# Performance work log

Hardware: AMD Instinct MI355X
Metric: run time of the kernel (lower is better)

The kernel has to match this reference:

```python
import jax, jax.numpy as jnp
import numpy as np
from jax import lax

B, L, H, I, Z = 1024, 128, 256, 32, 128  # batch, max_length, hidden, input_size, latent


def setup_inputs() -> dict:
    key = jax.random.key(0)
    ks = jax.random.split(key, 32)
    p = lambda k, shape: (jax.random.normal(k, shape, dtype=jnp.float32) * 0.05)
    d = {
        "x": jax.random.normal(ks[0], (B, Z), dtype=jnp.float32),
        "W1": p(ks[1], (512, Z)), "b1": p(ks[2], (512,)),
        "W2": p(ks[3], (512, 512)), "b2": p(ks[4], (512,)),
        "W3": p(ks[5], (512, 512)), "b3": p(ks[6], (512,)),
        # predict_h / predict_c / predict_x_0 heads
        "Wh1": p(ks[7], (512, 512)), "bh1": p(ks[8], (512,)),
        "Wh2": p(ks[9], (H, 512)), "bh2": p(ks[10], (H,)),
        "Wc1": p(ks[11], (512, 512)), "bc1": p(ks[12], (512,)),
        "Wc2": p(ks[13], (H, 512)), "bc2": p(ks[14], (H,)),
        "Wx1": p(ks[15], (512, 512)), "bx1": p(ks[16], (512,)),
        "Wx2": p(ks[17], (H, 512)), "bx2": p(ks[18], (H,)),
        # decode LSTM (input H -> hidden H), PyTorch gate order i,f,g,o
        "rWih": p(ks[19], (4 * H, H)), "rWhh": p(ks[20], (4 * H, H)),
        "rbih": p(ks[21], (4 * H,)), "rbhh": p(ks[22], (4 * H,)),
        # predictor LSTM (input H -> hidden I)
        "pWih": p(ks[23], (4 * I, H)), "pWhh": p(ks[24], (4 * I, I)),
        "pbih": p(ks[25], (4 * I,)), "pbhh": p(ks[26], (4 * I,)),
    }
    return d


def _leaky(v):
    return jnp.where(v >= 0, v, 0.2 * v)


def _lstm_cell(xt, h, c, Wih, Whh, b):
    gates = xt @ Wih.T + h @ Whh.T + b  # [B, 4G]
    i, f, g, o = jnp.split(gates, 4, axis=-1)
    c_new = jax.nn.sigmoid(f) * c + jax.nn.sigmoid(i) * jnp.tanh(g)
    h_new = jax.nn.sigmoid(o) * jnp.tanh(c_new)
    return h_new, c_new


def _forward(x, W1, b1, W2, b2, W3, b3, Wh1, bh1, Wh2, bh2, Wc1, bc1, Wc2, bc2,
             Wx1, bx1, Wx2, bx2, rWih, rWhh, rbih, rbhh, pWih, pWhh, pbih, pbhh):
    t = _leaky(x @ W1.T + b1)
    t = _leaky(t @ W2.T + b2)
    t = _leaky(t @ W3.T + b3)
    h = _leaky(t @ Wh1.T + bh1) @ Wh2.T + bh2   # [B, H]
    c = _leaky(t @ Wc1.T + bc1) @ Wc2.T + bc2   # [B, H]
    x0 = _leaky(t @ Wx1.T + bx1) @ Wx2.T + bx2  # [B, H]

    rb = rbih + rbhh
    # The torch loop re-feeds the growing sequence through the LSTM from the
    # same initial (h, c) each step; deterministically this equals a single
    # O(L) self-feeding scan: token_{i} = h-output of step i, fed at step i+1.
    def dec_step(carry, _):
        tok, hh, cc = carry
        h2, c2 = _lstm_cell(tok, hh, cc, rWih, rWhh, rb)
        return (h2, h2, c2), h2

    _, outs = lax.scan(dec_step, (x0, h, c), None, length=L)  # [L, B, H]

    pb = pbih + pbhh
    def pred_step(carry, xt):
        hh, cc = carry
        hh, cc = _lstm_cell(xt, hh, cc, pWih, pWhh, pb)
        return (hh, cc), hh

    h0 = jnp.zeros((B, I), dtype=x.dtype)
    _, pouts = lax.scan(pred_step, (h0, h0), outs)  # [L, B, I]
    y = jnp.transpose(pouts, (1, 0, 2))  # [B, L, I]

    layer_type = jax.nn.softmax(y[..., : I - 1], axis=-1)
    features = jax.nn.sigmoid(y[..., I - 1:])
    return jnp.concatenate([layer_type, features], axis=-1)


def reference(x, W1, b1, W2, b2, W3, b3, Wh1, bh1, Wh2, bh2, Wc1, bc1, Wc2, bc2,
              Wx1, bx1, Wx2, bx2, rWih, rWhh, rbih, rbhh, pWih, pWhh, pbih, pbhh):
    return _forward(x, W1, b1, W2, b2, W3, b3, Wh1, bh1, Wh2, bh2, Wc1, bc1, Wc2, bc2,
                    Wx1, bx1, Wx2, bx2, rWih, rWhh, rbih, rbhh, pWih, pWhh, pbih, pbhh)
```

## Files before the change

kernel.cpp:

```cpp
#include <hip/hip_runtime.h>
#include <hip/hip_fp8.h>

typedef unsigned short u16;
typedef unsigned char u8;
typedef __attribute__((ext_vector_type(8))) __bf16 bfrag;
typedef long long f8frag;
typedef __attribute__((ext_vector_type(4))) float f32x4;

static __device__ __forceinline__ f32x4 MFMA(bfrag a, bfrag b, f32x4 c) {
  return __builtin_amdgcn_mfma_f32_16x16x32_bf16(a, b, c, 0, 0, 0);
}
static __device__ __forceinline__ f32x4 MFMA8(f8frag a, f8frag b, f32x4 c) {
  return __builtin_amdgcn_mfma_f32_16x16x32_fp8_fp8(a, b, c, 0, 0, 0);
}

static __device__ __forceinline__ u16 f2b(float f) {
  union { float f; unsigned u; } v; v.f = f;
  unsigned r = (v.u + 0x7fffu + ((v.u >> 16) & 1u)) >> 16;
  return (u16)r;
}
static __device__ __forceinline__ u8 f2e4m3(float f) {
  return (u8)(__builtin_amdgcn_cvt_pk_fp8_f32(f, f, 0, false) & 0xff);
}
static __device__ __forceinline__ unsigned pk4_e4m3(float a, float b, float c, float d) {
  int p = __builtin_amdgcn_cvt_pk_fp8_f32(a, b, 0, false);
  p = __builtin_amdgcn_cvt_pk_fp8_f32(c, d, p, true);
  return (unsigned)p;
}
static __device__ __forceinline__ float rcp(float x) { return __builtin_amdgcn_rcpf(x); }
static __device__ __forceinline__ float ssig(float x) {
  float E = __expf(x);
  return E * rcp(1.f + E);
}
static __device__ __forceinline__ float2 lstm2(float gi, float gf, float gg,
                                               float go, float c) {
  float Ei = __expf(gi), Ef = __expf(gf), Eg = __expf(2.f * gg), Eo = __expf(go);
  float P = 1.f + Ef, Q = 1.f + Ei, R = 1.f + Eg;
  float QR = Q * R;
  float num = c * Ef * QR + Ei * P * (Eg - 1.f);
  float cn = num * rcp(P * QR);
  float Ec = __expf(2.f * cn);
  float hn = Eo * (Ec - 1.f) * rcp((1.f + Eo) * (Ec + 1.f));
  return make_float2(hn, cn);
}

#define LDS_BARRIER() asm volatile("s_waitcnt lgkmcnt(0)\ns_barrier" ::: "memory")
#define PIN_A8(A) asm volatile("" : "+a"(A[0]), "+a"(A[1]), "+a"(A[2]), "+a"(A[3]), \
                                    "+a"(A[4]), "+a"(A[5]), "+a"(A[6]), "+a"(A[7]))
#define PIN_V8(A) asm volatile("" : "+v"(A[0]), "+v"(A[1]), "+v"(A[2]), "+v"(A[3]), \
                                    "+v"(A[4]), "+v"(A[5]), "+v"(A[6]), "+v"(A[7]))

struct PrepArgs {
  const float *x, *W1, *W2, *W3, *Wh1, *Wc1, *Wx1, *Wh2, *Wc2, *Wx2;
  const float *rWih, *rWhh, *rbih, *rbhh, *pWih, *pWhh, *pbih, *pbhh;
  u16 *Xbf, *W1b, *W2b, *W3b, *Wh1b, *Wc1b, *Wx1b, *Wh2b, *Wc2b, *Wx2b;
  u16 *WcatR;
  u8 *WsS, *pWsS, *pWhhS;
  float *rbR, *pbR;
  unsigned *flags;
};

static __device__ __forceinline__ void emit_stream(u16* dst, const float* src,
                                                   int i, int K, int ktbits) {
  int j = i & 7, lane = (i >> 3) & 63;
  int kt = (i >> 9) & ((1 << ktbits) - 1);
  int nt = (i >> (9 + ktbits)) & 3;
  int ct = i >> (11 + ktbits);
  int srow = ct * 64 + nt * 16 + (lane & 15);
  int scol = kt * 32 + ((lane >> 4) & 3) * 8 + j;
  dst[i] = f2b(src[srow * K + scol]);
}

__global__ __launch_bounds__(256) void prep(PrepArgs p) {
  const int tid0 = blockIdx.x * 256 + threadIdx.x;
  const int stride = gridDim.x * 256;
  switch (blockIdx.y) {
    case 0: for (int i = tid0; i < 131072; i += stride) p.Xbf[i] = f2b(p.x[i]); break;
    case 1: for (int i = tid0; i < 65536;  i += stride) emit_stream(p.W1b, p.W1, i, 128, 2); break;
    case 2: for (int i = tid0; i < 262144; i += stride) emit_stream(p.W2b, p.W2, i, 512, 4); break;
    case 3: for (int i = tid0; i < 262144; i += stride) emit_stream(p.W3b, p.W3, i, 512, 4); break;
    case 4: for (int i = tid0; i < 262144; i += stride) emit_stream(p.Wh1b, p.Wh1, i, 512, 4); break;
    case 5: for (int i = tid0; i < 262144; i += stride) emit_stream(p.Wc1b, p.Wc1, i, 512, 4); break;
    case 6: for (int i = tid0; i < 262144; i += stride) emit_stream(p.Wx1b, p.Wx1, i, 512, 4); break;
    case 7: for (int i = tid0; i < 131072; i += stride) emit_stream(p.Wh2b, p.Wh2, i, 512, 4); break;
    case 8: for (int i = tid0; i < 131072; i += stride) emit_stream(p.Wc2b, p.Wc2, i, 512, 4); break;
    case 9: for (int i = tid0; i < 131072; i += stride) emit_stream(p.Wx2b, p.Wx2, i, 512, 4); break;
    case 10:
      for (int i = tid0; i < 524288; i += stride) {
        int j = i & 7, lane = (i >> 3) & 63, kt = (i >> 9) & 15;
        int gate = (i >> 13) & 3, w16 = i >> 15;
        int srow = gate * 256 + w16 * 16 + (lane & 15);
        int k = kt * 32 + ((lane >> 4) & 3) * 8 + j;
        float v = (k < 256) ? p.rWih[srow * 256 + k] : p.rWhh[srow * 256 + (k - 256)];
        p.WcatR[i] = f2b(v);
      }
      break;
    case 11:
      for (int i = tid0; i < 1024; i += stride) {
        int srow = (((i >> 4) & 3) << 8) + ((i >> 6) << 4) + (i & 15);
        p.rbR[i] = p.rbih[srow] + p.rbhh[srow];
      }
      break;
    case 12:
      for (int i = tid0; i < 32768; i += stride) {
        int j = i & 7, lane = (i >> 3) & 63, kt = (i >> 9) & 7, w = i >> 12;
        int n = w * 16 + (lane & 15);
        int srow = ((n & 3) << 5) + (n >> 2);
        int k = kt * 32 + ((lane >> 4) & 3) * 8 + j;
        p.pWsS[i] = f2e4m3(p.pWih[srow * 256 + k]);
      }
      break;
    case 13:
      for (int i = tid0; i < 4096; i += stride) {
        int j = i & 7, lane = (i >> 3) & 63, w = i >> 9;
        int n = w * 16 + (lane & 15);
        int srow = ((n & 3) << 5) + (n >> 2);
        int k = ((lane >> 4) & 3) * 8 + j;
        p.pWhhS[i] = f2e4m3(p.pWhh[srow * 32 + k]);
      }
      break;
    case 14:
      for (int i = tid0; i < 128; i += stride) {
        int srow = ((i & 3) << 5) + (i >> 2);
        p.pbR[i] = p.pbih[srow] + p.pbhh[srow];
      }
      for (int i = tid0; i < 64; i += stride)
        __hip_atomic_store(p.flags + i, 0u, __ATOMIC_RELAXED, __HIP_MEMORY_SCOPE_AGENT);
      break;
    case 15:
      for (int i = tid0; i < 262144; i += stride) {
        int j = i & 7, lane = (i >> 3) & 63, kt = (i >> 9) & 7;
        int gate = (i >> 12) & 3, g16 = i >> 14;
        int srow = gate * 256 + g16 * 16 + (lane & 15);
        int k = kt * 32 + ((lane >> 4) & 3) * 8 + j;
        p.WsS[i] = f2e4m3(p.rWih[srow * 256 + k] + p.rWhh[srow * 256 + k]);
      }
      break;
  }
}

__global__ __launch_bounds__(256) void gemm_act(
    const u16* __restrict__ X, const u16* __restrict__ W,
    const float* __restrict__ bias,
    u16* __restrict__ Yb, float* __restrict__ Yf,
    int K, int ldo, int coloff, int leaky) {
  const int rt = blockIdx.x, ct = blockIdx.y;
  const int lane = threadIdx.x & 63, wave = threadIdx.x >> 6;
  const int m15 = lane & 15, q = lane >> 4, kq = q * 8;
  const int KT = K >> 5;
  const int row = rt * 64 + wave * 16 + m15;
  f32x4 acc[4] = {};
  const u16* xp = X + (size_t)row * K + kq;
  const u16* wst = W + lane * 8;
  for (int kt = 0; kt < KT; kt++) {
    bfrag a = *(const bfrag*)(xp + kt * 32);
#pragma unroll
    for (int nt = 0; nt < 4; nt++) {
      const u16* wp = wst + (size_t)((ct * 4 + nt) * KT + kt) * 512;
      acc[nt] = MFMA(a, *(const bfrag*)wp, acc[nt]);
    }
  }
#pragma unroll
  for (int nt = 0; nt < 4; nt++) {
    int col = ct * 64 + nt * 16 + m15;
    float bv = bias[col];
#pragma unroll
    for (int r = 0; r < 4; r++) {
      int orow = rt * 64 + wave * 16 + q * 4 + r;
      float v = acc[nt][r] + bv;
      if (leaky) v = v >= 0.f ? v : 0.2f * v;
      if (Yb) Yb[(size_t)orow * ldo + coloff + col] = f2b(v);
      else    Yf[(size_t)orow * ldo + coloff + col] = v;
    }
  }
}

struct G3 {
  const u16 *X, *W;
  const float* bias;
  u16* Yb;
  float* Yf;
  int K, ldo, coloff, leaky;
};
__global__ __launch_bounds__(256) void gemm_act3(G3 ga, G3 gb, G3 gc) {
  G3 g = (blockIdx.z == 0) ? ga : (blockIdx.z == 1) ? gb : gc;
  const int rt = blockIdx.x, ct = blockIdx.y;
  const int lane = threadIdx.x & 63, wave = threadIdx.x >> 6;
  const int m15 = lane & 15, q = lane >> 4, kq = q * 8;
  const int KT = g.K >> 5;
  const int row = rt * 64 + wave * 16 + m15;
  f32x4 acc[4] = {};
  const u16* xp = g.X + (size_t)row * g.K + kq;
  const u16* wst = g.W + lane * 8;
  for (int kt = 0; kt < KT; kt++) {
    bfrag a = *(const bfrag*)(xp + kt * 32);
#pragma unroll
    for (int nt = 0; nt < 4; nt++) {
      const u16* wp = wst + (size_t)((ct * 4 + nt) * KT + kt) * 512;
      acc[nt] = MFMA(a, *(const bfrag*)wp, acc[nt]);
    }
  }
#pragma unroll
  for (int nt = 0; nt < 4; nt++) {
    int col = ct * 64 + nt * 16 + m15;
    float bv = g.bias[col];
#pragma unroll
    for (int r = 0; r < 4; r++) {
      int orow = rt * 64 + wave * 16 + q * 4 + r;
      float v = acc[nt][r] + bv;
      if (g.leaky) v = v >= 0.f ? v : 0.2f * v;
      if (g.Yb) g.Yb[(size_t)orow * g.ldo + g.coloff + col] = f2b(v);
      else      g.Yf[(size_t)orow * g.ldo + g.coloff + col] = v;
    }
  }
}

__global__ __attribute__((amdgpu_flat_work_group_size(1024, 1024), amdgpu_waves_per_eu(4, 4)))
void decode_pred(
    const u8* __restrict__ WsS,
    const u16* __restrict__ WcatR,
    const float* __restrict__ rb,
    const float* __restrict__ CB,
    const u16* __restrict__ X0H,
    const u8* __restrict__ pWsS,
    const u8* __restrict__ pWhhS,
    const float* __restrict__ pb,
    float* __restrict__ out,
    u8* __restrict__ hG,
    unsigned* __restrict__ flags) {
  __shared__ __align__(16) u8 hbufS[2][4096];
  __shared__ __align__(16) u8 WoL[16][4096];
  __shared__ __align__(16) u8 stageL[16384];
  __shared__ __align__(16) u8 hp8[2][16][40];
  __shared__ float ysC[4][16][36];
  const int tid = threadIdx.x;
  const int w = tid >> 6, lane = tid & 63;
  const int m15 = lane & 15, q = lane >> 4;

  if (blockIdx.x < 64) {
    const int b = blockIdx.x;
    const int rowg = b * 16;
    {
      int4* dst = (int4*)WoL;
      for (int i = tid; i < 4096; i += 1024) {
        int wv = i >> 8, rest = i & 255;
        dst[i] = ((const int4*)(WsS + wv * 16384 + 12288))[rest];
      }
    }
    const float* rbp = rb + w * 64 + q * 4;
    f32x4 rbv0 = *(const f32x4*)(rbp +  0);
    f32x4 rbv1 = *(const f32x4*)(rbp + 16);
    f32x4 rbv2 = *(const f32x4*)(rbp + 32);
    f32x4 rbv3 = *(const f32x4*)(rbp + 48);
    asm volatile("" : "+v"(rbv0), "+v"(rbv1), "+v"(rbv2), "+v"(rbv3));
    f32x4 cst = *(const f32x4*)(CB + (size_t)(rowg + m15) * 256 + w * 16 + q * 4);
    const int wroff = (w >> 1) * 512 + ((w & 1) * 2 + (q >> 1)) * 128 + m15 * 8 + (q & 1) * 4;
    u8* hGs = hG + (size_t)b * 524288 + wroff;

    {
      f32x4 ai = rbv0, af_ = rbv1, ag = rbv2, ao = rbv3;
      const u16* xrow = X0H + (size_t)(rowg + m15) * 512 + q * 8;
      const u16* wcw = WcatR + (size_t)w * 32768 + lane * 8;
#pragma unroll
      for (int kt = 0; kt < 16; kt++) {
        bfrag a = *(const bfrag*)(xrow + kt * 32);
        ai  = MFMA(*(const bfrag*)(wcw + kt * 512), a, ai);
        af_ = MFMA(*(const bfrag*)(wcw + 8192 + kt * 512), a, af_);
        ag  = MFMA(*(const bfrag*)(wcw + 16384 + kt * 512), a, ag);
        ao  = MFMA(*(const bfrag*)(wcw + 24576 + kt * 512), a, ao);
      }
      float hn[4];
#pragma unroll
      for (int r = 0; r < 4; r++) {
        float2 hc2 = lstm2(ai[r], af_[r], ag[r], ao[r], cst[r]);
        hn[r] = hc2.x;
        cst[r] = hc2.y;
      }
      unsigned hv = pk4_e4m3(hn[0], hn[1], hn[2], hn[3]);
      *(unsigned*)(&hbufS[0][wroff]) = hv;
      __hip_atomic_store((unsigned*)hGs, hv, __ATOMIC_RELAXED, __HIP_MEMORY_SCOPE_AGENT);
    }
    const u8* wsb = WsS + (size_t)w * 16384 + lane * 8;
    f8frag Wv0[8], Wv1[8], Wv2[8];
#pragma unroll
    for (int kt = 0; kt < 8; kt++) {
      Wv0[kt] = *(const f8frag*)(wsb + kt * 512);
      Wv1[kt] = *(const f8frag*)(wsb + 4096 + kt * 512);
      Wv2[kt] = *(const f8frag*)(wsb + 8192 + kt * 512);
    }
    PIN_A8(Wv0); PIN_A8(Wv1); PIN_A8(Wv2);
    const u8* woW = &WoL[w][lane * 8];
    __syncthreads();

    for (int s = 1; s < 128; s++) {
      PIN_A8(Wv0); PIN_A8(Wv1); PIN_A8(Wv2);
      asm volatile("" : "+v"(rbv0), "+v"(rbv1), "+v"(rbv2), "+v"(rbv3));
      const u8* h8 = &hbufS[(s - 1) & 1][lane * 8];
      f32x4 ai = rbv0, af_ = rbv1, ag = rbv2, ao = rbv3;
#pragma unroll
      for (int kt = 0; kt < 8; kt++) {
        f8frag a8 = *(const f8frag*)(h8 + kt * 512);
        f8frag wo = *(const f8frag*)(woW + kt * 512);
        ai  = MFMA8(Wv0[kt], a8, ai);
        af_ = MFMA8(Wv1[kt], a8, af_);
        ag  = MFMA8(Wv2[kt], a8, ag);
        ao  = MFMA8(wo, a8, ao);
      }
      float hn[4];
#pragma unroll
      for (int r = 0; r < 4; r++) {
        float2 hc2 = lstm2(ai[r], af_[r], ag[r], ao[r], cst[r]);
        hn[r] = hc2.x;
        cst[r] = hc2.y;
      }
      unsigned hv = pk4_e4m3(hn[0], hn[1], hn[2], hn[3]);
      *(unsigned*)(&hbufS[s & 1][wroff]) = hv;
      __hip_atomic_store((unsigned*)(hGs + (size_t)s * 4096), hv,
                         __ATOMIC_RELAXED, __HIP_MEMORY_SCOPE_AGENT);
      if ((s & 3) == 3) {
        __syncthreads();
        if (tid == 0)
          __hip_atomic_store(flags + b, (unsigned)((s >> 2) + 1),
                             __ATOMIC_RELEASE, __HIP_MEMORY_SCOPE_AGENT);
      } else {
        LDS_BARRIER();
      }
    }
  } else {
    const int b = blockIdx.x - 64;
    const int rowg = b * 16;
    for (int i = tid; i < 2 * 16 * 40; i += 1024) (&hp8[0][0][0])[i] = 0;
    const u8* pwsb = pWsS + (size_t)(w & 7) * 4096 + lane * 8;
    f8frag pbv[8];
#pragma unroll
    for (int kt = 0; kt < 8; kt++) pbv[kt] = *(const f8frag*)(pwsb + kt * 512);
    f8frag phw = *(const f8frag*)(pWhhS + (size_t)(w & 7) * 512 + lane * 8);
    PIN_V8(pbv);
    asm volatile("" : "+v"(phw));
    const f32x4 pbias = *(const f32x4*)(pb + (w & 7) * 16 + q * 4);
    float cp = 0.f;
    const u8* hGc = hG + (size_t)b * 524288;
    const int t_si = (tid >> 3) >> 4, t_r = (tid >> 3) & 15, sub = tid & 7;

    for (int cs = 0; cs < 32; cs++) {
      if (tid == 0) {
        while (__hip_atomic_load(flags + b, __ATOMIC_ACQUIRE,
                                 __HIP_MEMORY_SCOPE_AGENT) < (unsigned)(cs + 1))
          __builtin_amdgcn_s_sleep(2);
      }
      __syncthreads();
      {
        const unsigned* src = (const unsigned*)(hGc + (size_t)cs * 16384) + tid * 4;
        unsigned d0 = __hip_atomic_load(src + 0, __ATOMIC_RELAXED, __HIP_MEMORY_SCOPE_AGENT);
        unsigned d1 = __hip_atomic_load(src + 1, __ATOMIC_RELAXED, __HIP_MEMORY_SCOPE_AGENT);
        unsigned d2 = __hip_atomic_load(src + 2, __ATOMIC_RELAXED, __HIP_MEMORY_SCOPE_AGENT);
        unsigned d3 = __hip_atomic_load(src + 3, __ATOMIC_RELAXED, __HIP_MEMORY_SCOPE_AGENT);
        int4 vv; vv.x = d0; vv.y = d1; vv.z = d2; vv.w = d3;
        *(int4*)&stageL[tid * 16] = vv;
      }
      __syncthreads();
#pragma unroll
      for (int si = 0; si < 4; si++) {
        const int s = cs * 4 + si;
        if (w < 8) {
          const u8* xr8 = &stageL[si * 4096 + lane * 8];
          f32x4 pacc = pbias;
#pragma unroll
          for (int kt = 0; kt < 8; kt++) {
            f8frag pav = *(const f8frag*)(xr8 + kt * 512);
            pacc = MFMA8(pbv[kt], pav, pacc);
          }
          f8frag pah = *(const f8frag*)(&hp8[s & 1][m15][q * 8]);
          pacc = MFMA8(phw, pah, pacc);
          float2 hc2 = lstm2(pacc[0], pacc[1], pacc[2], pacc[3], cp);
          cp = hc2.y;
          hp8[(s + 1) & 1][m15][w * 4 + q] = f2e4m3(hc2.x);
          ysC[si][m15][w * 4 + q] = hc2.x;
        }
        LDS_BARRIER();
      }
      if (tid < 512) {
        f32x4 yv = *(const f32x4*)&ysC[t_si][t_r][sub * 4];
        float v3 = (sub == 7) ? -1e30f : yv[3];
        float m = fmaxf(fmaxf(yv[0], yv[1]), fmaxf(yv[2], v3));
#pragma unroll
        for (int off = 4; off; off >>= 1) m = fmaxf(m, __shfl_xor(m, off, 8));
        float e0 = __expf(yv[0] - m), e1 = __expf(yv[1] - m), e2 = __expf(yv[2] - m);
        float e3 = (sub == 7) ? 0.f : __expf(yv[3] - m);
        float tot = e0 + e1 + e2 + e3;
#pragma unroll
        for (int off = 4; off; off >>= 1) tot += __shfl_xor(tot, off, 8);
        float inv = rcp(tot);
        f32x4 o;
        o[0] = e0 * inv; o[1] = e1 * inv; o[2] = e2 * inv;
        o[3] = (sub == 7) ? ssig(yv[3]) : e3 * inv;
        *(f32x4*)(out + (size_t)(rowg + t_r) * 4096 + (cs * 4 + t_si) * 32 + sub * 4) = o;
      }
      LDS_BARRIER();
    }
  }
}

extern "C" void kernel_launch(void* const* d_in, const int* in_sizes, int n_in,
                              void* d_out, int out_size, void* d_ws, size_t ws_size,
                              hipStream_t stream) {
  (void)in_sizes; (void)n_in; (void)out_size; (void)ws_size;
  const float* x    = (const float*)d_in[0];
  const float* W1   = (const float*)d_in[1];
  const float* b1   = (const float*)d_in[2];
  const float* W2   = (const float*)d_in[3];
  const float* b2   = (const float*)d_in[4];
  const float* W3   = (const float*)d_in[5];
  const float* b3   = (const float*)d_in[6];
  const float* Wh1  = (const float*)d_in[7];
  const float* bh1  = (const float*)d_in[8];
  const float* Wh2  = (const float*)d_in[9];
  const float* bh2  = (const float*)d_in[10];
  const float* Wc1  = (const float*)d_in[11];
  const float* bc1  = (const float*)d_in[12];
  const float* Wc2  = (const float*)d_in[13];
  const float* bc2  = (const float*)d_in[14];
  const float* Wx1  = (const float*)d_in[15];
  const float* bx1  = (const float*)d_in[16];
  const float* Wx2  = (const float*)d_in[17];
  const float* bx2  = (const float*)d_in[18];
  const float* rWih = (const float*)d_in[19];
  const float* rWhh = (const float*)d_in[20];
  const float* rbih = (const float*)d_in[21];
  const float* rbhh = (const float*)d_in[22];
  const float* pWih = (const float*)d_in[23];
  const float* pWhh = (const float*)d_in[24];
  const float* pbih = (const float*)d_in[25];
  const float* pbhh = (const float*)d_in[26];

  char* w = (char*)d_ws;
  auto alloc = [&](size_t bytes) -> char* {
    char* p = w;
    w += (bytes + 255) & ~(size_t)255;
    return p;
  };
  u16* Xbf  = (u16*)alloc(1024 * 128 * 2);
  u16* T1   = (u16*)alloc(1024 * 512 * 2);
  u16* T2   = (u16*)alloc(1024 * 512 * 2);
  u16* T3   = (u16*)alloc(1024 * 512 * 2);
  u16* TH   = (u16*)alloc(1024 * 512 * 2);
  u16* TC   = (u16*)alloc(1024 * 512 * 2);
  u16* TX   = (u16*)alloc(1024 * 512 * 2);
  u16* X0H  = (u16*)alloc(1024 * 512 * 2);
  float* CB = (float*)alloc(1024 * 256 * 4);
  u16* W1b  = (u16*)alloc(512 * 128 * 2);
  u16* W2b  = (u16*)alloc(512 * 512 * 2);
  u16* W3b  = (u16*)alloc(512 * 512 * 2);
  u16* Wh1b = (u16*)alloc(512 * 512 * 2);
  u16* Wc1b = (u16*)alloc(512 * 512 * 2);
  u16* Wx1b = (u16*)alloc(512 * 512 * 2);
  u16* Wh2b = (u16*)alloc(256 * 512 * 2);
  u16* Wc2b = (u16*)alloc(256 * 512 * 2);
  u16* Wx2b = (u16*)alloc(256 * 512 * 2);
  u16* WcatR= (u16*)alloc(1024 * 512 * 2);
  u8*  WsS  = (u8*)alloc(262144);
  u8*  pWsS = (u8*)alloc(32768);
  u8*  pWhhS= (u8*)alloc(4096);
  float* rbR = (float*)alloc(1024 * 4);
  float* pbR = (float*)alloc(128 * 4);
  unsigned* flags = (unsigned*)alloc(64 * 4);
  u8*  hG   = (u8*)alloc((size_t)64 * 128 * 4096);

  PrepArgs pa;
  pa.x = x; pa.W1 = W1; pa.W2 = W2; pa.W3 = W3; pa.Wh1 = Wh1; pa.Wc1 = Wc1; pa.Wx1 = Wx1;
  pa.Wh2 = Wh2; pa.Wc2 = Wc2; pa.Wx2 = Wx2;
  pa.rWih = rWih; pa.rWhh = rWhh; pa.rbih = rbih; pa.rbhh = rbhh;
  pa.pWih = pWih; pa.pWhh = pWhh; pa.pbih = pbih; pa.pbhh = pbhh;
  pa.Xbf = Xbf; pa.W1b = W1b; pa.W2b = W2b; pa.W3b = W3b; pa.Wh1b = Wh1b;
  pa.Wc1b = Wc1b; pa.Wx1b = Wx1b; pa.Wh2b = Wh2b; pa.Wc2b = Wc2b; pa.Wx2b = Wx2b;
  pa.WcatR = WcatR;
  pa.WsS = WsS; pa.pWsS = pWsS; pa.pWhhS = pWhhS;
  pa.rbR = rbR; pa.pbR = pbR;
  pa.flags = flags;
  prep<<<dim3(32, 16), 256, 0, stream>>>(pa);

  gemm_act<<<dim3(16, 8), 256, 0, stream>>>(Xbf, W1b, b1, T1, nullptr, 128, 512, 0, 1);
  gemm_act<<<dim3(16, 8), 256, 0, stream>>>(T1, W2b, b2, T2, nullptr, 512, 512, 0, 1);
  gemm_act<<<dim3(16, 8), 256, 0, stream>>>(T2, W3b, b3, T3, nullptr, 512, 512, 0, 1);
  G3 h1a = {T3, Wh1b, bh1, TH, nullptr, 512, 512, 0, 1};
  G3 h1b = {T3, Wc1b, bc1, TC, nullptr, 512, 512, 0, 1};
  G3 h1c = {T3, Wx1b, bx1, TX, nullptr, 512, 512, 0, 1};
  gemm_act3<<<dim3(16, 8, 3), 256, 0, stream>>>(h1a, h1b, h1c);
  G3 h2a = {TH, Wh2b, bh2, X0H, nullptr, 512, 512, 256, 0};
  G3 h2b = {TC, Wc2b, bc2, nullptr, CB, 512, 256, 0, 0};
  G3 h2c = {TX, Wx2b, bx2, X0H, nullptr, 512, 512, 0, 0};
  gemm_act3<<<dim3(16, 4, 3), 256, 0, stream>>>(h2a, h2b, h2c);

  decode_pred<<<128, 1024, 0, stream>>>(WsS, WcatR, rbR, CB, X0H,
                                        pWsS, pWhhS, pbR,
                                        (float*)d_out, hG, flags);
}
```

Baseline: 459.0 us.

## Fuse MLP GEMM chain into one persistent kernel and batch decode flags by eight

Replaces the five separate GEMM launches with one persistent kernel of 128 blocks that runs all MLP layers, separated by a software grid barrier on an atomic counter. This removes per-launch overhead and tail gaps between the dependent small GEMMs. The decode-to-predictor handoff now signals every eight steps instead of four, with a doubled staging buffer, which halves the flag polling and barrier traffic. The cost is a longer wait before the predictor can start each chunk. The grid barrier is only safe if all 128 blocks are resident at the same time, and it adds spin cost.

Result: slower. 502.4 us (+9.5%).

```diff
diff --git a/kernel.cpp b/kernel.cpp
--- a/kernel.cpp
+++ b/kernel.cpp
@@ -124,7 +124,7 @@
         int srow = ((i & 3) << 5) + (i >> 2);
         p.pbR[i] = p.pbih[srow] + p.pbhh[srow];
       }
-      for (int i = tid0; i < 64; i += stride)
+      for (int i = tid0; i < 72; i += stride)
         __hip_atomic_store(p.flags + i, 0u, __ATOMIC_RELAXED, __HIP_MEMORY_SCOPE_AGENT);
       break;
     case 15:
@@ -139,13 +139,12 @@
   }
 }
 
-__global__ __launch_bounds__(256) void gemm_act(
+static __device__ void gemm_tile(
     const u16* __restrict__ X, const u16* __restrict__ W,
     const float* __restrict__ bias,
     u16* __restrict__ Yb, float* __restrict__ Yf,
-    int K, int ldo, int coloff, int leaky) {
-  const int rt = blockIdx.x, ct = blockIdx.y;
-  const int lane = threadIdx.x & 63, wave = threadIdx.x >> 6;
+    int K, int ldo, int coloff, int leaky, int rt, int ct, int tid) {
+  const int lane = tid & 63, wave = tid >> 6;
   const int m15 = lane & 15, q = lane >> 4, kq = q * 8;
   const int KT = K >> 5;
   const int row = rt * 64 + wave * 16 + m15;
@@ -175,42 +174,47 @@
   }
 }
 
-struct G3 {
-  const u16 *X, *W;
-  const float* bias;
-  u16* Yb;
-  float* Yf;
-  int K, ldo, coloff, leaky;
+static __device__ __forceinline__ void grid_bar(unsigned* bar, unsigned target) {
+  __syncthreads();
+  if (threadIdx.x == 0) {
+    __threadfence();
+    __hip_atomic_fetch_add(bar, 1u, __ATOMIC_ACQ_REL, __HIP_MEMORY_SCOPE_AGENT);
+    while (__hip_atomic_load(bar, __ATOMIC_ACQUIRE, __HIP_MEMORY_SCOPE_AGENT) < target)
+      __builtin_amdgcn_s_sleep(1);
+    __threadfence();
+  }
+  __syncthreads();
+}
+
+struct MlpArgs {
+  const u16 *Xbf, *W1b, *W2b, *W3b, *Wh1b, *Wh2b, *Wc1b, *Wc2b, *Wx1b, *Wx2b;
+  const float *b1, *b2, *b3, *bh1, *bh2, *bc1, *bc2, *bx1, *bx2;
+  u16 *T1, *T2, *T3, *TH, *TC, *TX, *X0H;
+  float* CB;
+  unsigned* bar;
 };
-__global__ __launch_bounds__(256) void gemm_act3(G3 ga, G3 gb, G3 gc) {
-  G3 g = (blockIdx.z == 0) ? ga : (blockIdx.z == 1) ? gb : gc;
-  const int rt = blockIdx.x, ct = blockIdx.y;
-  const int lane = threadIdx.x & 63, wave = threadIdx.x >> 6;
-  const int m15 = lane & 15, q = lane >> 4, kq = q * 8;
-  const int KT = g.K >> 5;
-  const int row = rt * 64 + wave * 16 + m15;
-  f32x4 acc[4] = {};
-  const u16* xp = g.X + (size_t)row * g.K + kq;
-  const u16* wst = g.W + lane * 8;
-  for (int kt = 0; kt < KT; kt++) {
-    bfrag a = *(const bfrag*)(xp + kt * 32);
-#pragma unroll
-    for (int nt = 0; nt < 4; nt++) {
-      const u16* wp = wst + (size_t)((ct * 4 + nt) * KT + kt) * 512;
-      acc[nt] = MFMA(a, *(const bfrag*)wp, acc[nt]);
-    }
-  }
-#pragma unroll
-  for (int nt = 0; nt < 4; nt++) {
-    int col = ct * 64 + nt * 16 + m15;
-    float bv = g.bias[col];
-#pragma unroll
-    for (int r = 0; r < 4; r++) {
-      int orow = rt * 64 + wave * 16 + q * 4 + r;
-      float v = acc[nt][r] + bv;
-      if (g.leaky) v = v >= 0.f ? v : 0.2f * v;
-      if (g.Yb) g.Yb[(size_t)orow * g.ldo + g.coloff + col] = f2b(v);
-      else      g.Yf[(size_t)orow * g.ldo + g.coloff + col] = v;
+
+__global__ __launch_bounds__(256) void fused_mlp(MlpArgs a) {
+  const int blk = blockIdx.x, tid = threadIdx.x;
+  const int rt = blk >> 3, ct = blk & 7;
+  gemm_tile(a.Xbf, a.W1b, a.b1, a.T1, nullptr, 128, 512, 0, 1, rt, ct, tid);
+  grid_bar(a.bar, 128);
+  gemm_tile(a.T1, a.W2b, a.b2, a.T2, nullptr, 512, 512, 0, 1, rt, ct, tid);
+  grid_bar(a.bar, 256);
+  gemm_tile(a.T2, a.W3b, a.b3, a.T3, nullptr, 512, 512, 0, 1, rt, ct, tid);
+  grid_bar(a.bar, 384);
+  gemm_tile(a.T3, a.Wh1b, a.bh1, a.TH, nullptr, 512, 512, 0, 1, rt, ct, tid);
+  gemm_tile(a.T3, a.Wc1b, a.bc1, a.TC, nullptr, 512, 512, 0, 1, rt, ct, tid);
+  gemm_tile(a.T3, a.Wx1b, a.bx1, a.TX, nullptr, 512, 512, 0, 1, rt, ct, tid);
+  grid_bar(a.bar, 512);
+  {
+    int t = blk;
+    int job = t >> 6, tile = t & 63, rt2 = tile >> 2, ct2 = tile & 3;
+    if (job == 0)      gemm_tile(a.TH, a.Wh2b, a.bh2, a.X0H, nullptr, 512, 512, 256, 0, rt2, ct2, tid);
+    else               gemm_tile(a.TC, a.Wc2b, a.bc2, nullptr, a.CB, 512, 256, 0, 0, rt2, ct2, tid);
+    if (blk < 64) {
+      int tile2 = (128 + blk) & 63, rt3 = tile2 >> 2, ct3 = tile2 & 3;
+      gemm_tile(a.TX, a.Wx2b, a.bx2, a.X0H, nullptr, 512, 512, 0, 0, rt3, ct3, tid);
     }
   }
 }
@@ -230,9 +234,9 @@
     unsigned* __restrict__ flags) {
   __shared__ __align__(16) u8 hbufS[2][4096];
   __shared__ __align__(16) u8 WoL[16][4096];
-  __shared__ __align__(16) u8 stageL[16384];
+  __shared__ __align__(16) u8 stageL[32768];
   __shared__ __align__(16) u8 hp8[2][16][40];
-  __shared__ float ysC[4][16][36];
+  __shared__ float ysC[8][16][36];
   const int tid = threadIdx.x;
   const int w = tid >> 6, lane = tid & 63;
   const int m15 = lane & 15, q = lane >> 4;
@@ -317,10 +321,10 @@
       *(unsigned*)(&hbufS[s & 1][wroff]) = hv;
       __hip_atomic_store((unsigned*)(hGs + (size_t)s * 4096), hv,
                          __ATOMIC_RELAXED, __HIP_MEMORY_SCOPE_AGENT);
-      if ((s & 3) == 3) {
+      if ((s & 7) == 7) {
         __syncthreads();
         if (tid == 0)
-          __hip_atomic_store(flags + b, (unsigned)((s >> 2) + 1),
+          __hip_atomic_store(flags + b, (unsigned)((s >> 3) + 1),
                              __ATOMIC_RELEASE, __HIP_MEMORY_SCOPE_AGENT);
       } else {
         LDS_BARRIER();
@@ -342,7 +346,7 @@
     const u8* hGc = hG + (size_t)b * 524288;
     const int t_si = (tid >> 3) >> 4, t_r = (tid >> 3) & 15, sub = tid & 7;
 
-    for (int cs = 0; cs < 32; cs++) {
+    for (int cs = 0; cs < 16; cs++) {
       if (tid == 0) {
         while (__hip_atomic_load(flags + b, __ATOMIC_ACQUIRE,
                                  __HIP_MEMORY_SCOPE_AGENT) < (unsigned)(cs + 1))
@@ -350,18 +354,22 @@
       }
       __syncthreads();
       {
-        const unsigned* src = (const unsigned*)(hGc + (size_t)cs * 16384) + tid * 4;
-        unsigned d0 = __hip_atomic_load(src + 0, __ATOMIC_RELAXED, __HIP_MEMORY_SCOPE_AGENT);
-        unsigned d1 = __hip_atomic_load(src + 1, __ATOMIC_RELAXED, __HIP_MEMORY_SCOPE_AGENT);
-        unsigned d2 = __hip_atomic_load(src + 2, __ATOMIC_RELAXED, __HIP_MEMORY_SCOPE_AGENT);
-        unsigned d3 = __hip_atomic_load(src + 3, __ATOMIC_RELAXED, __HIP_MEMORY_SCOPE_AGENT);
-        int4 vv; vv.x = d0; vv.y = d1; vv.z = d2; vv.w = d3;
-        *(int4*)&stageL[tid * 16] = vv;
+        const unsigned* src = (const unsigned*)(hGc + (size_t)cs * 32768) + tid * 4;
+#pragma unroll
+        for (int hh = 0; hh < 2; hh++) {
+          unsigned d0 = __hip_atomic_load(src + 0, __ATOMIC_RELAXED, __HIP_MEMORY_SCOPE_AGENT);
+          unsigned d1 = __hip_atomic_load(src + 1, __ATOMIC_RELAXED, __HIP_MEMORY_SCOPE_AGENT);
+          unsigned d2 = __hip_atomic_load(src + 2, __ATOMIC_RELAXED, __HIP_MEMORY_SCOPE_AGENT);
+          unsigned d3 = __hip_atomic_load(src + 3, __ATOMIC_RELAXED, __HIP_MEMORY_SCOPE_AGENT);
+          int4 vv; vv.x = d0; vv.y = d1; vv.z = d2; vv.w = d3;
+          *(int4*)&stageL[tid * 16 + hh * 16384] = vv;
+          src += 4096;
+        }
       }
       __syncthreads();
 #pragma unroll
-      for (int si = 0; si < 4; si++) {
-        const int s = cs * 4 + si;
+      for (int si = 0; si < 8; si++) {
+        const int s = cs * 8 + si;
         if (w < 8) {
           const u8* xr8 = &stageL[si * 4096 + lane * 8];
           f32x4 pacc = pbias;
@@ -379,7 +387,7 @@
         }
         LDS_BARRIER();
       }
-      if (tid < 512) {
+      {
         f32x4 yv = *(const f32x4*)&ysC[t_si][t_r][sub * 4];
         float v3 = (sub == 7) ? -1e30f : yv[3];
         float m = fmaxf(fmaxf(yv[0], yv[1]), fmaxf(yv[2], v3));
@@ -394,7 +402,7 @@
         f32x4 o;
         o[0] = e0 * inv; o[1] = e1 * inv; o[2] = e2 * inv;
         o[3] = (sub == 7) ? ssig(yv[3]) : e3 * inv;
-        *(f32x4*)(out + (size_t)(rowg + t_r) * 4096 + (cs * 4 + t_si) * 32 + sub * 4) = o;
+        *(f32x4*)(out + (size_t)(rowg + t_r) * 4096 + (cs * 8 + t_si) * 32 + sub * 4) = o;
       }
       LDS_BARRIER();
     }
@@ -463,7 +471,7 @@
   u8*  pWhhS= (u8*)alloc(4096);
   float* rbR = (float*)alloc(1024 * 4);
   float* pbR = (float*)alloc(128 * 4);
-  unsigned* flags = (unsigned*)alloc(64 * 4);
+  unsigned* flags = (unsigned*)alloc(72 * 4);
   u8*  hG   = (u8*)alloc((size_t)64 * 128 * 4096);
 
   PrepArgs pa;
@@ -479,17 +487,16 @@
   pa.flags = flags;
   prep<<<dim3(32, 16), 256, 0, stream>>>(pa);
 
-  gemm_act<<<dim3(16, 8), 256, 0, stream>>>(Xbf, W1b, b1, T1, nullptr, 128, 512, 0, 1);
-  gemm_act<<<dim3(16, 8), 256, 0, stream>>>(T1, W2b, b2, T2, nullptr, 512, 512, 0, 1);
-  gemm_act<<<dim3(16, 8), 256, 0, stream>>>(T2, W3b, b3, T3, nullptr, 512, 512, 0, 1);
-  G3 h1a = {T3, Wh1b, bh1, TH, nullptr, 512, 512, 0, 1};
-  G3 h1b = {T3, Wc1b, bc1, TC, nullptr, 512, 512, 0, 1};
-  G3 h1c = {T3, Wx1b, bx1, TX, nullptr, 512, 512, 0, 1};
-  gemm_act3<<<dim3(16, 8, 3), 256, 0, stream>>>(h1a, h1b, h1c);
-  G3 h2a = {TH, Wh2b, bh2, X0H, nullptr, 512, 512, 256, 0};
-  G3 h2b = {TC, Wc2b, bc2, nullptr, CB, 512, 256, 0, 0};
-  G3 h2c = {TX, Wx2b, bx2, X0H, nullptr, 512, 512, 0, 0};
-  gemm_act3<<<dim3(16, 4, 3), 256, 0, stream>>>(h2a, h2b, h2c);
+  MlpArgs ml;
+  ml.Xbf = Xbf; ml.W1b = W1b; ml.W2b = W2b; ml.W3b = W3b;
+  ml.Wh1b = Wh1b; ml.Wh2b = Wh2b; ml.Wc1b = Wc1b; ml.Wc2b = Wc2b;
+  ml.Wx1b = Wx1b; ml.Wx2b = Wx2b;
+  ml.b1 = b1; ml.b2 = b2; ml.b3 = b3; ml.bh1 = bh1; ml.bh2 = bh2;
+  ml.bc1 = bc1; ml.bc2 = bc2; ml.bx1 = bx1; ml.bx2 = bx2;
+  ml.T1 = T1; ml.T2 = T2; ml.T3 = T3; ml.TH = TH; ml.TC = TC; ml.TX = TX;
+  ml.X0H = X0H; ml.CB = CB;
+  ml.bar = flags + 64;
+  fused_mlp<<<128, 256, 0, stream>>>(ml);
 
   decode_pred<<<128, 1024, 0, stream>>>(WsS, WcatR, rbR, CB, X0H,
                                         pWsS, pWhhS, pbR,
```
